# Kernel tuning notes

Hardware: AMD Instinct MI355X
Metric: run time of the kernel (lower is better)

The kernel has to match this reference:

```python
import jax, jax.numpy as jnp
import numpy as np
import math

NHEADS = 16
CAUSAL = True
NEG_INF = -1e18


def setup_inputs() -> dict:
    key = jax.random.key(0)
    kq, kk, kv = jax.random.split(key, 3)
    B, S, D = 4, 8192, 1024
    q = jax.random.normal(kq, (B, S, D), dtype=jnp.float32)
    k = jax.random.normal(kk, (B, S, D), dtype=jnp.float32)
    v = jax.random.normal(kv, (B, S, D), dtype=jnp.float32)
    return {"q": q, "k": k, "v": v}


def reference(q, k, v):
    # Faithful to the torch code: it views (B,S,H*hd)->(B,S,H,hd) WITHOUT
    # transposing heads to dim 1, so matmul(q, k^T) is an (H,H) score matrix
    # per token -- attention across HEADS, causal mask/softmax over heads.
    B, S, D = q.shape
    hd = D // NHEADS
    qh = q.reshape(B, S, NHEADS, hd)
    kh = k.reshape(B, S, NHEADS, hd)
    vh = v.reshape(B, S, NHEADS, hd)
    # scores: (B, S, H, H)
    scores = jnp.einsum('bsqd,bskd->bsqk', qh, kh) / math.sqrt(hd)
    if CAUSAL:
        mask = jnp.tril(jnp.ones((NHEADS, NHEADS), dtype=bool))
        scores = jnp.where(mask, scores, jnp.asarray(NEG_INF, scores.dtype))
    attn = jax.nn.softmax(scores, axis=-1)
    out = jnp.einsum('bsqk,bskd->bsqd', attn, vh)
    return out.reshape(B, S, D)
```

## Files before the change

kernel.cpp:

```cpp
#include <hip/hip_runtime.h>
#include <math.h>

#define DMODEL 1024
#define TOKW 4

typedef _Float16 f16x4 __attribute__((ext_vector_type(4)));
typedef _Float16 f16x8 __attribute__((ext_vector_type(8)));
typedef float    f32x4 __attribute__((ext_vector_type(4)));

__global__ __launch_bounds__(256) void temporal_attn_kernel(
    const float* __restrict__ q,
    const float* __restrict__ k,
    const float* __restrict__ v,
    float* __restrict__ out)
{
    const int lane = threadIdx.x & 63;
    const int wave = threadIdx.x >> 6;
    const int r = lane & 15;
    const int G = lane >> 4;
    const size_t base = ((size_t)blockIdx.x * TOKW + wave) * DMODEL;

    const float* qrow = q + base + r * 64;
    const float* krow = k + base + r * 64;
    f32x4 ql[4], kl[4];
#pragma unroll
    for (int c = 0; c < 2; ++c)
#pragma unroll
        for (int h = 0; h < 2; ++h) {
            ql[2 * c + h] = *(const f32x4*)(qrow + 32 * c + 8 * G + 4 * h);
            kl[2 * c + h] = *(const f32x4*)(krow + 32 * c + 8 * G + 4 * h);
        }
    float vl[4][4];
#pragma unroll
    for (int t = 0; t < 4; ++t)
#pragma unroll
        for (int cg = 0; cg < 4; ++cg)
            vl[t][cg] = v[base + (size_t)(4 * G + t) * 64 + 16 * cg + r];

    f16x8 ka[2], qb[2];
#pragma unroll
    for (int c = 0; c < 2; ++c)
#pragma unroll
        for (int h = 0; h < 2; ++h)
#pragma unroll
            for (int e = 0; e < 4; ++e) {
                ka[c][4 * h + e] = (_Float16)kl[2 * c + h][e];
                qb[c][4 * h + e] = (_Float16)ql[2 * c + h][e];
            }

    f32x4 acc = {0.f, 0.f, 0.f, 0.f};
    acc = __builtin_amdgcn_mfma_f32_16x16x32_f16(ka[0], qb[0], acc, 0, 0, 0);
    acc = __builtin_amdgcn_mfma_f32_16x16x32_f16(ka[1], qb[1], acc, 0, 0, 0);

    float s[4];
#pragma unroll
    for (int e = 0; e < 4; ++e) {
        const int j = 4 * G + e;
        s[e] = (j > r) ? -1e30f : acc[e] * 0.125f;
    }
    float m = fmaxf(fmaxf(s[0], s[1]), fmaxf(s[2], s[3]));
    m = fmaxf(m, __shfl_xor(m, 16));
    m = fmaxf(m, __shfl_xor(m, 32));
    const float e0 = __expf(s[0] - m);
    const float e1 = __expf(s[1] - m);
    const float e2 = __expf(s[2] - m);
    const float e3 = __expf(s[3] - m);
    float sum = e0 + e1 + e2 + e3;
    sum += __shfl_xor(sum, 16);
    sum += __shfl_xor(sum, 32);
    const float inv = 1.0f / sum;
    f16x4 pa;
    pa[0] = (_Float16)(e0 * inv);
    pa[1] = (_Float16)(e1 * inv);
    pa[2] = (_Float16)(e2 * inv);
    pa[3] = (_Float16)(e3 * inv);

#pragma unroll
    for (int cg = 0; cg < 4; ++cg) {
        f16x4 vb;
#pragma unroll
        for (int t = 0; t < 4; ++t) vb[t] = (_Float16)vl[t][cg];
        f32x4 o = {0.f, 0.f, 0.f, 0.f};
        o = __builtin_amdgcn_mfma_f32_16x16x16f16(pa, vb, o, 0, 0, 0);
        float* obase = out + base + (size_t)(4 * G) * 64 + 16 * cg + r;
#pragma unroll
        for (int e = 0; e < 4; ++e)
            obase[e * 64] = o[e];
    }
}

extern "C" void kernel_launch(void* const* d_in, const int* in_sizes, int n_in,
                              void* d_out, int out_size, void* d_ws, size_t ws_size,
                              hipStream_t stream) {
    const float* q = (const float*)d_in[0];
    const float* k = (const float*)d_in[1];
    const float* v = (const float*)d_in[2];
    float* o = (float*)d_out;
    const int ntok = in_sizes[0] / DMODEL;
    temporal_attn_kernel<<<ntok / TOKW, 256, 0, stream>>>(q, k, v, o);
}
```

Before: 96.89 us.

## Use persistent grid-stride kernel with register double-buffered token loads

Launches a fixed grid of 1024 blocks that loop over tokens with a grid stride. Each iteration prefetches the next token's q/k/v into a second register set before computing and storing the current one, to overlap memory latency with compute. Output stores become nontemporal to avoid polluting cache. Doubling the live registers may reduce occupancy, and the fixed grid may underfill the device or unbalance work.

Result: slower. 99.89 us (+3.1%).

```diff
diff --git a/kernel.cpp b/kernel.cpp
--- a/kernel.cpp
+++ b/kernel.cpp
@@ -3,26 +3,20 @@
 
 #define DMODEL 1024
 #define TOKW 4
+#define NBLK 1024
 
 typedef _Float16 f16x4 __attribute__((ext_vector_type(4)));
 typedef _Float16 f16x8 __attribute__((ext_vector_type(8)));
 typedef float    f32x4 __attribute__((ext_vector_type(4)));
 
-__global__ __launch_bounds__(256) void temporal_attn_kernel(
-    const float* __restrict__ q,
-    const float* __restrict__ k,
-    const float* __restrict__ v,
-    float* __restrict__ out)
+__device__ __forceinline__ void load_tok(const float* __restrict__ q,
+                                         const float* __restrict__ k,
+                                         const float* __restrict__ v,
+                                         size_t base, int r, int G,
+                                         f32x4 ql[4], f32x4 kl[4], float vl[4][4])
 {
-    const int lane = threadIdx.x & 63;
-    const int wave = threadIdx.x >> 6;
-    const int r = lane & 15;
-    const int G = lane >> 4;
-    const size_t base = ((size_t)blockIdx.x * TOKW + wave) * DMODEL;
-
     const float* qrow = q + base + r * 64;
     const float* krow = k + base + r * 64;
-    f32x4 ql[4], kl[4];
 #pragma unroll
     for (int c = 0; c < 2; ++c)
 #pragma unroll
@@ -30,13 +24,18 @@
             ql[2 * c + h] = *(const f32x4*)(qrow + 32 * c + 8 * G + 4 * h);
             kl[2 * c + h] = *(const f32x4*)(krow + 32 * c + 8 * G + 4 * h);
         }
-    float vl[4][4];
 #pragma unroll
     for (int t = 0; t < 4; ++t)
 #pragma unroll
         for (int cg = 0; cg < 4; ++cg)
             vl[t][cg] = v[base + (size_t)(4 * G + t) * 64 + 16 * cg + r];
+}
 
+__device__ __forceinline__ void compute_store(float* __restrict__ out,
+                                              size_t base, int r, int G,
+                                              const f32x4 ql[4], const f32x4 kl[4],
+                                              const float vl[4][4])
+{
     f16x8 ka[2], qb[2];
 #pragma unroll
     for (int c = 0; c < 2; ++c)
@@ -85,7 +84,47 @@
         float* obase = out + base + (size_t)(4 * G) * 64 + 16 * cg + r;
 #pragma unroll
         for (int e = 0; e < 4; ++e)
-            obase[e * 64] = o[e];
+            __builtin_nontemporal_store(o[e], obase + e * 64);
+    }
+}
+
+__global__ __launch_bounds__(256, 3) void temporal_attn_kernel(
+    const float* __restrict__ q,
+    const float* __restrict__ k,
+    const float* __restrict__ v,
+    float* __restrict__ out,
+    int ntok)
+{
+    const int lane = threadIdx.x & 63;
+    const int wave = threadIdx.x >> 6;
+    const int r = lane & 15;
+    const int G = lane >> 4;
+    const int W = gridDim.x * TOKW;
+    int t0 = blockIdx.x * TOKW + wave;
+    if (t0 >= ntok) return;
+
+    f32x4 qA[4], kA[4], qB[4], kB[4];
+    float vA[4][4], vB[4][4];
+
+    load_tok(q, k, v, (size_t)t0 * DMODEL, r, G, qA, kA, vA);
+    for (;;) {
+        const int t1 = t0 + W;
+        if (t1 < ntok) {
+            load_tok(q, k, v, (size_t)t1 * DMODEL, r, G, qB, kB, vB);
+            compute_store(out, (size_t)t0 * DMODEL, r, G, qA, kA, vA);
+            const int t2 = t1 + W;
+            if (t2 < ntok) {
+                load_tok(q, k, v, (size_t)t2 * DMODEL, r, G, qA, kA, vA);
+                compute_store(out, (size_t)t1 * DMODEL, r, G, qB, kB, vB);
+                t0 = t2;
+            } else {
+                compute_store(out, (size_t)t1 * DMODEL, r, G, qB, kB, vB);
+                break;
+            }
+        } else {
+            compute_store(out, (size_t)t0 * DMODEL, r, G, qA, kA, vA);
+            break;
+        }
     }
 }
 
@@ -97,5 +136,5 @@
     const float* v = (const float*)d_in[2];
     float* o = (float*)d_out;
     const int ntok = in_sizes[0] / DMODEL;
-    temporal_attn_kernel<<<ntok / TOKW, 256, 0, stream>>>(q, k, v, o);
+    temporal_attn_kernel<<<NBLK, 256, 0, stream>>>(q, k, v, o, ntok);
 }
```

## Use persistent single-wave blocks with double-buffered direct-to-LDS async loads

Applied to the files above, without the earlier changes.

Replaces the one-token-per-wave grid with a persistent grid of 1536 single-wave blocks that loop over tokens with a stride. The q, k and v rows are staged into a double-buffered LDS region through global_load_lds DMA, with an XOR swizzle on q and k to avoid bank conflicts. Hand-placed vmcnt waits let the next token's loads overlap compute on the current one. The intent is to hide global memory latency in this bandwidth-bound kernel, at the cost of fragile manual waitcnt accounting and fewer waves in flight.

New measurement: 106.4 us. 9.8% more time.

```diff
diff --git a/kernel.cpp b/kernel.cpp
--- a/kernel.cpp
+++ b/kernel.cpp
@@ -2,55 +2,58 @@
 #include <math.h>
 
 #define DMODEL 1024
-#define TOKW 4
+#define NBLK   1536
+#define BUF_F  3072
 
 typedef _Float16 f16x4 __attribute__((ext_vector_type(4)));
 typedef _Float16 f16x8 __attribute__((ext_vector_type(8)));
 typedef float    f32x4 __attribute__((ext_vector_type(4)));
 
-__global__ __launch_bounds__(256) void temporal_attn_kernel(
-    const float* __restrict__ q,
-    const float* __restrict__ k,
-    const float* __restrict__ v,
-    float* __restrict__ out)
+__device__ __forceinline__ void dma16(const float* g, float* l) {
+    __builtin_amdgcn_global_load_lds(
+        (const __attribute__((address_space(1))) void*)g,
+        (__attribute__((address_space(3))) void*)l, 16, 0, 0);
+}
+
+__device__ __forceinline__ void stage_tok(const float* __restrict__ q,
+                                          const float* __restrict__ k,
+                                          const float* __restrict__ v,
+                                          size_t tbase, float* buf, int lane)
 {
-    const int lane = threadIdx.x & 63;
-    const int wave = threadIdx.x >> 6;
-    const int r = lane & 15;
-    const int G = lane >> 4;
-    const size_t base = ((size_t)blockIdx.x * TOKW + wave) * DMODEL;
+#pragma unroll
+    for (int i = 0; i < 4; ++i) {
+        const int s  = 64 * i + lane;
+        const int rr = s >> 4;
+        const int oo = (s & 15) ^ (rr & 7);
+        const int go = rr * 64 + oo * 4;
+        dma16(q + tbase + go, buf + 256 * i);
+        dma16(k + tbase + go, buf + 1024 + 256 * i);
+        dma16(v + tbase + 256 * i + 4 * lane, buf + 2048 + 256 * i);
+    }
+}
 
-    const float* qrow = q + base + r * 64;
-    const float* krow = k + base + r * 64;
-    f32x4 ql[4], kl[4];
+__device__ __forceinline__ void compute_store(float* __restrict__ out, size_t tbase,
+                                              const float* buf, int r, int G)
+{
+    const int r7 = r & 7;
+    f16x8 ka[2], qa[2];
 #pragma unroll
     for (int c = 0; c < 2; ++c)
 #pragma unroll
         for (int h = 0; h < 2; ++h) {
-            ql[2 * c + h] = *(const f32x4*)(qrow + 32 * c + 8 * G + 4 * h);
-            kl[2 * c + h] = *(const f32x4*)(krow + 32 * c + 8 * G + 4 * h);
-        }
-    float vl[4][4];
-#pragma unroll
-    for (int t = 0; t < 4; ++t)
-#pragma unroll
-        for (int cg = 0; cg < 4; ++cg)
-            vl[t][cg] = v[base + (size_t)(4 * G + t) * 64 + 16 * cg + r];
-
-    f16x8 ka[2], qb[2];
-#pragma unroll
-    for (int c = 0; c < 2; ++c)
-#pragma unroll
-        for (int h = 0; h < 2; ++h)
+            const int slot = (8 * c + 2 * G + h) ^ r7;
+            const f32x4 qf = *(const f32x4*)(buf +        r * 64 + 4 * slot);
+            const f32x4 kf = *(const f32x4*)(buf + 1024 + r * 64 + 4 * slot);
 #pragma unroll
             for (int e = 0; e < 4; ++e) {
-                ka[c][4 * h + e] = (_Float16)kl[2 * c + h][e];
-                qb[c][4 * h + e] = (_Float16)ql[2 * c + h][e];
+                qa[c][4 * h + e] = (_Float16)qf[e];
+                ka[c][4 * h + e] = (_Float16)kf[e];
             }
+        }
 
     f32x4 acc = {0.f, 0.f, 0.f, 0.f};
-    acc = __builtin_amdgcn_mfma_f32_16x16x32_f16(ka[0], qb[0], acc, 0, 0, 0);
-    acc = __builtin_amdgcn_mfma_f32_16x16x32_f16(ka[1], qb[1], acc, 0, 0, 0);
+    acc = __builtin_amdgcn_mfma_f32_16x16x32_f16(ka[0], qa[0], acc, 0, 0, 0);
+    acc = __builtin_amdgcn_mfma_f32_16x16x32_f16(ka[1], qa[1], acc, 0, 0, 0);
 
     float s[4];
 #pragma unroll
@@ -75,17 +78,56 @@
     pa[2] = (_Float16)(e2 * inv);
     pa[3] = (_Float16)(e3 * inv);
 
+    const float* vb = buf + 2048;
 #pragma unroll
     for (int cg = 0; cg < 4; ++cg) {
-        f16x4 vb;
+        f16x4 vf;
 #pragma unroll
-        for (int t = 0; t < 4; ++t) vb[t] = (_Float16)vl[t][cg];
+        for (int t_ = 0; t_ < 4; ++t_)
+            vf[t_] = (_Float16)vb[(4 * G + t_) * 64 + 16 * cg + r];
         f32x4 o = {0.f, 0.f, 0.f, 0.f};
-        o = __builtin_amdgcn_mfma_f32_16x16x16f16(pa, vb, o, 0, 0, 0);
-        float* obase = out + base + (size_t)(4 * G) * 64 + 16 * cg + r;
+        o = __builtin_amdgcn_mfma_f32_16x16x16f16(pa, vf, o, 0, 0, 0);
+        float* obase = out + tbase + (size_t)(4 * G) * 64 + 16 * cg + r;
 #pragma unroll
         for (int e = 0; e < 4; ++e)
             obase[e * 64] = o[e];
+    }
+}
+
+__global__ __launch_bounds__(64) void temporal_attn_kernel(
+    const float* __restrict__ q,
+    const float* __restrict__ k,
+    const float* __restrict__ v,
+    float* __restrict__ out, int ntok)
+{
+    __shared__ float smem[2 * BUF_F];
+    const int lane = threadIdx.x;
+    const int r = lane & 15;
+    const int G = lane >> 4;
+    const int S = NBLK;
+    int t = blockIdx.x;
+    if (t >= ntok) return;
+
+    stage_tok(q, k, v, (size_t)t * DMODEL, smem, lane);
+    if (t + S < ntok)
+        stage_tok(q, k, v, (size_t)(t + S) * DMODEL, smem + BUF_F, lane);
+    asm volatile("s_waitcnt vmcnt(12)" ::: "memory");
+    __builtin_amdgcn_sched_barrier(0);
+
+    int cur = 0;
+    for (; t < ntok; t += S) {
+        float* buf = (float*)smem + cur * BUF_F;
+        compute_store(out, (size_t)t * DMODEL, buf, r, G);
+        __builtin_amdgcn_sched_barrier(0);
+        if (t + 2 * S < ntok) {
+            stage_tok(q, k, v, (size_t)(t + 2 * S) * DMODEL, buf, lane);
+            __builtin_amdgcn_sched_barrier(0);
+            asm volatile("s_waitcnt vmcnt(28)" ::: "memory");
+        } else if (t + S < ntok) {
+            asm volatile("s_waitcnt vmcnt(16)" ::: "memory");
+        }
+        __builtin_amdgcn_sched_barrier(0);
+        cur ^= 1;
     }
 }
 
@@ -97,5 +139,5 @@
     const float* v = (const float*)d_in[2];
     float* o = (float*)d_out;
     const int ntok = in_sizes[0] / DMODEL;
-    temporal_attn_kernel<<<ntok / TOKW, 256, 0, stream>>>(q, k, v, o);
+    temporal_attn_kernel<<<NBLK, 64, 0, stream>>>(q, k, v, o, ntok);
 }
```
